# Kernel tuning notes

Measured on AMD Instinct MI355X. Metric: run time of the kernel, lower is better.

Reference implementation:

```python
import jax, jax.numpy as jnp
import numpy as np

N_PER_CLOUD = 2048   # points per cloud (batch entries are equal-sized, sorted)
NUM_CLOUDS = 8       # batch_size constant in the source module
RADIUS = 0.2         # init arg r
MAX_NEIGHBORS = 32   # init arg max_neighbors
F_IN, H1, H2, F_OUT = 3, 64, 64, 128  # PointNet++ SA MLP widths; nn input = F_IN + 3


def setup_inputs() -> dict:
    key = jax.random.key(0)
    ks = jax.random.split(key, 8)
    N = NUM_CLOUDS * N_PER_CLOUD
    x = jax.random.normal(ks[0], (N, F_IN), dtype=jnp.float32)
    pos = jax.random.uniform(ks[1], (N, 3), dtype=jnp.float32)  # unit cube
    batch = jnp.repeat(jnp.arange(NUM_CLOUDS, dtype=jnp.int32), N_PER_CLOUD)
    d_in = F_IN + 3
    W1 = jax.random.normal(ks[2], (d_in, H1), dtype=jnp.float32) / np.sqrt(d_in)
    b1 = jnp.zeros((H1,), dtype=jnp.float32)
    W2 = jax.random.normal(ks[3], (H1, H2), dtype=jnp.float32) / np.sqrt(H1)
    b2 = jnp.zeros((H2,), dtype=jnp.float32)
    W3 = jax.random.normal(ks[4], (H2, F_OUT), dtype=jnp.float32) / np.sqrt(H2)
    b3 = jnp.zeros((F_OUT,), dtype=jnp.float32)
    return dict(x=x, pos=pos, batch=batch, W1=W1, b1=b1, W2=W2, b2=b2, W3=W3, b3=b3)


def reference(x, pos, batch, W1, b1, W2, b2, W3, b3):
    N = pos.shape[0]
    B = N // N_PER_CLOUD
    n = N_PER_CLOUD
    posb = pos.reshape(B, n, 3)
    xb = x.reshape(B, n, -1)

    # --- radius ball query (per cloud, first MAX_NEIGHBORS in index order) ---
    diff = posb[:, :, None, :] - posb[:, None, :, :]          # [B, n_query, n_src, 3]
    d2 = jnp.sum(diff * diff, axis=-1)                        # [B, n, n]
    valid = d2 <= RADIUS * RADIUS                             # includes self -> >=1 nbr
    j_idx = jnp.arange(n, dtype=jnp.int32)
    keys = jnp.where(valid, j_idx[None, None, :], n)          # invalid -> sentinel n
    nbr = jnp.argsort(keys, axis=-1)[..., :MAX_NEIGHBORS]     # [B, n, K]
    nbr_ok = jnp.take_along_axis(keys, nbr, axis=-1) < n      # [B, n, K] bool

    # --- PointNetConv: msg = nn(cat([x_j, pos_j - pos_i])), max aggregation ---
    b_ix = jnp.arange(B)[:, None, None]
    x_j = xb[b_ix, nbr]                                        # [B, n, K, F_IN]
    rel = posb[b_ix, nbr] - posb[:, :, None, :]               # [B, n, K, 3]
    msg = jnp.concatenate([x_j, rel], axis=-1)                # [B, n, K, F_IN+3]
    h = jax.nn.relu(msg @ W1 + b1)
    h = jax.nn.relu(h @ W2 + b2)
    h = h @ W3 + b3                                           # [B, n, K, F_OUT]
    h = jnp.where(nbr_ok[..., None], h, -jnp.inf)
    out = jnp.max(h, axis=2).reshape(N, -1)                   # [N, F_OUT]
    return out, pos, batch
```

## Files before the change

kernel.cpp:

```cpp
#include <hip/hip_runtime.h>
#include <hip/hip_bf16.h>
#include <math.h>

#define NPC   2048
#define NC    8
#define NTOT  (NPC * NC)
#define KMAX  32
#define R2    0.04f

typedef short bf16x8  __attribute__((ext_vector_type(8)));
typedef float f32x16  __attribute__((ext_vector_type(16)));

__device__ __forceinline__ unsigned int f2bf(float f) {
    unsigned int u = __float_as_uint(f);
    return (u + 0x7FFFu + ((u >> 16) & 1u)) >> 16;
}

__device__ __forceinline__ unsigned int pkbf(float a, float b) {
    unsigned int r;
    asm("v_cvt_pk_bf16_f32 %0, %1, %2" : "=v"(r) : "v"(a), "v"(b));
    return r;
}

__device__ __forceinline__ bf16x8 mk_frag(const f32x16& a, int off) {
    int4 w;
    w.x = (int)pkbf(fmaxf(a[off+0],0.f), fmaxf(a[off+1],0.f));
    w.y = (int)pkbf(fmaxf(a[off+2],0.f), fmaxf(a[off+3],0.f));
    w.z = (int)pkbf(fmaxf(a[off+4],0.f), fmaxf(a[off+5],0.f));
    w.w = (int)pkbf(fmaxf(a[off+6],0.f), fmaxf(a[off+7],0.f));
    return __builtin_bit_cast(bf16x8, w);
}

__global__ __launch_bounds__(512) void prep_kernel(
    const float* __restrict__ x, const float* __restrict__ pos,
    const int* __restrict__ batch,
    const float* __restrict__ W1, const float* __restrict__ b1,
    const float* __restrict__ W2, const float* __restrict__ b2,
    const float* __restrict__ W3,
    int* __restrict__ nbr, int* __restrict__ cnts,
    float* __restrict__ xp, unsigned short* __restrict__ wf,
    float* __restrict__ out)
{
    __shared__ float4 sP[NPC];

    int b = blockIdx.x, tid = threadIdx.x;
    if (b < 2048) {
        const int base = (b >> 8) << 11;
        #pragma unroll
        for (int p = tid; p < NPC; p += 512) {
            sP[p] = make_float4(pos[3*(base+p)], pos[3*(base+p)+1], pos[3*(base+p)+2], 0.f);
        }
        __syncthreads();

        const int lane = tid & 63;
        const int q    = b * 8 + (tid >> 6);
        float qx = pos[3*q], qy = pos[3*q+1], qz = pos[3*q+2];
        int cnt = 0;
        for (int j0 = 0; j0 < NPC && cnt < KMAX; j0 += 256) {
            unsigned long long ms[4];
            bool vs[4];
            #pragma unroll
            for (int s = 0; s < 4; ++s) {
                float4 p = sP[j0 + s*64 + lane];
                float dx = __fsub_rn(p.x, qx);
                float dy = __fsub_rn(p.y, qy);
                float dz = __fsub_rn(p.z, qz);
                float d2 = __fadd_rn(__fadd_rn(__fmul_rn(dx,dx), __fmul_rn(dy,dy)),
                                     __fmul_rn(dz,dz));
                vs[s] = d2 <= R2;
                ms[s] = __ballot(vs[s]);
            }
            #pragma unroll
            for (int s = 0; s < 4; ++s) {
                int before = (int)__popcll(ms[s] & ((1ull << lane) - 1ull));
                int slot = cnt + before;
                if (vs[s] && slot < KMAX) nbr[(q << 5) + slot] = base + j0 + s*64 + lane;
                cnt += (int)__popcll(ms[s]);
            }
        }
        if (lane == 0) cnts[q] = cnt < KMAX ? cnt : KMAX;
    } else if (b < 2080) {
        int i = (b - 2048) * 512 + tid;
        float4 v0 = {x[3*i], x[3*i+1], x[3*i+2], pos[3*i]};
        float4 v1 = {pos[3*i+1], pos[3*i+2], 0.f, 0.f};
        float4* dst = (float4*)(xp + 8 * i);
        dst[0] = v0; dst[1] = v1;
    } else if (b < 2108) {
        int g = (b - 2080) * 512 + tid;
        if (g < 1024) {
            int j = g & 7, lane = (g >> 3) & 63, t = g >> 9;
            int k = (lane >> 5)*8 + j, ch = t*32 + (lane & 31);
            float v = (k < 6) ? W1[k*64 + ch] : (k == 6 ? b1[ch] : 0.f);
            wf[g] = (unsigned short)f2bf(v);
        } else if (g < 6144) {
            int g2 = g - 1024;
            int j = g2 & 7, lane = (g2 >> 3) & 63, f = g2 >> 9;
            int t = f / 5, kk = f % 5;
            int hi = lane >> 5, row = t*32 + (lane & 31);
            float v;
            if (kk < 4) {
                int k = (j & 3) + 4*hi + 8*(2*(kk & 1) + (j >> 2)) + 32*(kk >> 1);
                v = W2[k*64 + row];
            } else {
                v = (hi == 0 && j == 0) ? b2[row] : 0.f;
            }
            wf[g] = (unsigned short)f2bf(v);
        } else {
            int g3 = g - 6144;
            int j = g3 & 7, lane = (g3 >> 3) & 63, f = g3 >> 9;
            int n = f >> 2, kk = f & 3;
            int hi = lane >> 5, col = n*32 + (lane & 31);
            int k = (j & 3) + 4*hi + 8*(2*(kk & 1) + (j >> 2)) + 32*(kk >> 1);
            wf[g] = (unsigned short)f2bf(W3[k*128 + col]);
        }
    } else {
        int i = (b - 2108) * 512 + tid;
        if (i < NTOT*3) out[NTOT*128 + i] = pos[i];
        if (i < NTOT)   out[NTOT*131 + i] = (float)batch[i];
    }
}

__global__ __launch_bounds__(256, 4) void mlp_kernel(
    const unsigned short* __restrict__ wf, const float* __restrict__ b3,
    const float* __restrict__ xp,
    const int* __restrict__ nbr, const int* __restrict__ cnts,
    float* __restrict__ out)
{
    __shared__ int4 sW[1664];

    const int tid  = threadIdx.x;
    const int lane = tid & 63, wave = tid >> 6;
    const int e = lane & 31, hi = lane >> 5;

    const int qq  = __builtin_amdgcn_readfirstlane(blockIdx.x * 4 + wave);
    const int cnt = cnts[qq];

    int jg = (e < cnt) ? nbr[(qq << 5) + e] : qq;
    const float4* pj = (const float4*)(xp + 8*jg);
    float4 xj0 = pj[0], xj1 = pj[1];
    float qpx = xp[8*qq + 3], qpy = xp[8*qq + 4], qpz = xp[8*qq + 5];

    bf16x8 wA1_0 = *(const bf16x8*)(wf + (0*64 + lane)*8);
    bf16x8 wA1_1 = *(const bf16x8*)(wf + (1*64 + lane)*8);

    float b3v[4];
    #pragma unroll
    for (int n = 0; n < 4; ++n) b3v[n] = b3[n*32 + e];

    const int4* wsrc = (const int4*)(wf + 1024);
    #pragma unroll
    for (int it = 0; it < 7; ++it) {
        int idx = it*256 + tid;
        if (idx < 1664) sW[idx] = wsrc[idx];
    }
    __syncthreads();

    const unsigned int one_w = pkbf(1.0f, 0.0f);
    int4 ow = {0,0,0,0};
    if (!hi) ow.x = (int)one_w;
    const bf16x8 onef = __builtin_bit_cast(bf16x8, ow);

    float r0 = xj0.w - qpx, r1 = xj1.x - qpy, r2 = xj1.y - qpz;
    int4 mw;
    mw.x = hi ? 0 : (int)pkbf(xj0.x, xj0.y);
    mw.y = hi ? 0 : (int)pkbf(xj0.z, r0);
    mw.z = hi ? 0 : (int)pkbf(r1, r2);
    mw.w = hi ? 0 : (int)one_w;
    bf16x8 msgf = __builtin_bit_cast(bf16x8, mw);

    f32x16 acc0 = {}, acc1 = {};
    acc0 = __builtin_amdgcn_mfma_f32_32x32x16_bf16(wA1_0, msgf, acc0, 0, 0, 0);
    acc1 = __builtin_amdgcn_mfma_f32_32x32x16_bf16(wA1_1, msgf, acc1, 0, 0, 0);
    bf16x8 h1f[4];
    h1f[0] = mk_frag(acc0, 0);
    h1f[1] = mk_frag(acc0, 8);
    h1f[2] = mk_frag(acc1, 0);
    h1f[3] = mk_frag(acc1, 8);

    f32x16 c20 = {}, c21 = {};
    #pragma unroll
    for (int kk = 0; kk < 4; ++kk) {
        c20 = __builtin_amdgcn_mfma_f32_32x32x16_bf16(
                *(const bf16x8*)&sW[(0*5 + kk)*64 + lane], h1f[kk], c20, 0, 0, 0);
        c21 = __builtin_amdgcn_mfma_f32_32x32x16_bf16(
                *(const bf16x8*)&sW[(1*5 + kk)*64 + lane], h1f[kk], c21, 0, 0, 0);
    }
    c20 = __builtin_amdgcn_mfma_f32_32x32x16_bf16(
            *(const bf16x8*)&sW[(0*5 + 4)*64 + lane], onef, c20, 0, 0, 0);
    c21 = __builtin_amdgcn_mfma_f32_32x32x16_bf16(
            *(const bf16x8*)&sW[(1*5 + 4)*64 + lane], onef, c21, 0, 0, 0);
    bf16x8 h2f[4];
    h2f[0] = mk_frag(c20, 0);
    h2f[1] = mk_frag(c20, 8);
    h2f[2] = mk_frag(c21, 0);
    h2f[3] = mk_frag(c21, 8);

    const bool full = (cnt == 32);
    #pragma unroll
    for (int n = 0; n < 4; ++n) {
        f32x16 c = {};
        #pragma unroll
        for (int kk = 0; kk < 4; ++kk)
            c = __builtin_amdgcn_mfma_f32_32x32x16_bf16(
                    h2f[kk], *(const bf16x8*)&sW[640 + (n*4 + kk)*64 + lane], c, 0, 0, 0);
        float m;
        if (full) {
            m = fmaxf(fmaxf(fmaxf(c[0],c[1]), fmaxf(c[2],c[3])),
                      fmaxf(fmaxf(c[4],c[5]), fmaxf(c[6],c[7])));
            m = fmaxf(m, fmaxf(fmaxf(c[8],c[9]),  fmaxf(c[10],c[11])));
            m = fmaxf(m, fmaxf(fmaxf(c[12],c[13]), fmaxf(c[14],c[15])));
        } else {
            m = -INFINITY;
            #pragma unroll
            for (int reg = 0; reg < 16; ++reg) {
                int r = (reg & 3) + 8*(reg >> 2) + 4*hi;
                float v = (r < cnt) ? c[reg] : -INFINITY;
                m = fmaxf(m, v);
            }
        }
        m = fmaxf(m, __shfl_xor(m, 32));
        m += b3v[n];
        if (hi == 0) out[qq*128 + n*32 + (lane & 31)] = m;
    }
}

extern "C" void kernel_launch(void* const* d_in, const int* in_sizes, int n_in,
                              void* d_out, int out_size, void* d_ws, size_t ws_size,
                              hipStream_t stream) {
    const float* x     = (const float*)d_in[0];
    const float* pos   = (const float*)d_in[1];
    const int*   batch = (const int*)d_in[2];
    const float* W1    = (const float*)d_in[3];
    const float* b1    = (const float*)d_in[4];
    const float* W2    = (const float*)d_in[5];
    const float* b2    = (const float*)d_in[6];
    const float* W3    = (const float*)d_in[7];
    const float* b3    = (const float*)d_in[8];
    float* out = (float*)d_out;

    int* nbr  = (int*)d_ws;
    int* cnts = nbr + NTOT * KMAX;
    float* xp = (float*)(cnts + NTOT);
    unsigned short* wfrag = (unsigned short*)(xp + NTOT*8);

    prep_kernel<<<2204, 512, 0, stream>>>(x, pos, batch, W1, b1, W2, b2, W3,
                                          nbr, cnts, xp, wfrag, out);
    mlp_kernel<<<NTOT / 4, 256, 0, stream>>>(wfrag, b3, xp, nbr, cnts, out);
}
```

Baseline: 38.44 us.

## Process two query points per wave to reuse weight fragments across MFMAs

Each wave now handles two query points instead of one. Every weight fragment loaded from LDS or global memory feeds two independent MFMA chains, and the grid is halved, so the per-block shared-memory weight staging is amortised over twice the work. The extra accumulators raise register pressure, so the launch-bounds occupancy hint drops from 4 to 3, which may reduce latency hiding.

Measured after the change: 36.75 us. 4.4% less time.

```diff
diff --git a/kernel.cpp b/kernel.cpp
--- a/kernel.cpp
+++ b/kernel.cpp
@@ -120,7 +120,7 @@
     }
 }
 
-__global__ __launch_bounds__(256, 4) void mlp_kernel(
+__global__ __launch_bounds__(256, 3) void mlp_kernel(
     const unsigned short* __restrict__ wf, const float* __restrict__ b3,
     const float* __restrict__ xp,
     const int* __restrict__ nbr, const int* __restrict__ cnts,
@@ -132,13 +132,16 @@
     const int lane = tid & 63, wave = tid >> 6;
     const int e = lane & 31, hi = lane >> 5;
 
-    const int qq  = __builtin_amdgcn_readfirstlane(blockIdx.x * 4 + wave);
-    const int cnt = cnts[qq];
-
-    int jg = (e < cnt) ? nbr[(qq << 5) + e] : qq;
-    const float4* pj = (const float4*)(xp + 8*jg);
-    float4 xj0 = pj[0], xj1 = pj[1];
-    float qpx = xp[8*qq + 3], qpy = xp[8*qq + 4], qpz = xp[8*qq + 5];
+    const int q0 = __builtin_amdgcn_readfirstlane(blockIdx.x * 8 + wave * 2);
+    const int q1 = q0 + 1;
+    const int cnt0 = cnts[q0], cnt1 = cnts[q1];
+
+    int jg0 = (e < cnt0) ? nbr[(q0 << 5) + e] : q0;
+    int jg1 = (e < cnt1) ? nbr[(q1 << 5) + e] : q1;
+    float4 a0 = ((const float4*)(xp + 8*jg0))[0], a1 = ((const float4*)(xp + 8*jg0))[1];
+    float4 c0 = ((const float4*)(xp + 8*jg1))[0], c1 = ((const float4*)(xp + 8*jg1))[1];
+    float p0x = xp[8*q0 + 3], p0y = xp[8*q0 + 4], p0z = xp[8*q0 + 5];
+    float p1x = xp[8*q1 + 3], p1y = xp[8*q1 + 4], p1z = xp[8*q1 + 5];
 
     bf16x8 wA1_0 = *(const bf16x8*)(wf + (0*64 + lane)*8);
     bf16x8 wA1_1 = *(const bf16x8*)(wf + (1*64 + lane)*8);
@@ -160,67 +163,96 @@
     if (!hi) ow.x = (int)one_w;
     const bf16x8 onef = __builtin_bit_cast(bf16x8, ow);
 
-    float r0 = xj0.w - qpx, r1 = xj1.x - qpy, r2 = xj1.y - qpz;
-    int4 mw;
-    mw.x = hi ? 0 : (int)pkbf(xj0.x, xj0.y);
-    mw.y = hi ? 0 : (int)pkbf(xj0.z, r0);
-    mw.z = hi ? 0 : (int)pkbf(r1, r2);
-    mw.w = hi ? 0 : (int)one_w;
-    bf16x8 msgf = __builtin_bit_cast(bf16x8, mw);
-
-    f32x16 acc0 = {}, acc1 = {};
-    acc0 = __builtin_amdgcn_mfma_f32_32x32x16_bf16(wA1_0, msgf, acc0, 0, 0, 0);
-    acc1 = __builtin_amdgcn_mfma_f32_32x32x16_bf16(wA1_1, msgf, acc1, 0, 0, 0);
-    bf16x8 h1f[4];
-    h1f[0] = mk_frag(acc0, 0);
-    h1f[1] = mk_frag(acc0, 8);
-    h1f[2] = mk_frag(acc1, 0);
-    h1f[3] = mk_frag(acc1, 8);
-
-    f32x16 c20 = {}, c21 = {};
+    int4 mw0, mw1;
+    mw0.x = hi ? 0 : (int)pkbf(a0.x, a0.y);
+    mw0.y = hi ? 0 : (int)pkbf(a0.z, a0.w - p0x);
+    mw0.z = hi ? 0 : (int)pkbf(a1.x - p0y, a1.y - p0z);
+    mw0.w = hi ? 0 : (int)one_w;
+    mw1.x = hi ? 0 : (int)pkbf(c0.x, c0.y);
+    mw1.y = hi ? 0 : (int)pkbf(c0.z, c0.w - p1x);
+    mw1.z = hi ? 0 : (int)pkbf(c1.x - p1y, c1.y - p1z);
+    mw1.w = hi ? 0 : (int)one_w;
+    bf16x8 msg0 = __builtin_bit_cast(bf16x8, mw0);
+    bf16x8 msg1 = __builtin_bit_cast(bf16x8, mw1);
+
+    f32x16 l0a = {}, l0b = {}, l1a = {}, l1b = {};
+    l0a = __builtin_amdgcn_mfma_f32_32x32x16_bf16(wA1_0, msg0, l0a, 0, 0, 0);
+    l1a = __builtin_amdgcn_mfma_f32_32x32x16_bf16(wA1_0, msg1, l1a, 0, 0, 0);
+    l0b = __builtin_amdgcn_mfma_f32_32x32x16_bf16(wA1_1, msg0, l0b, 0, 0, 0);
+    l1b = __builtin_amdgcn_mfma_f32_32x32x16_bf16(wA1_1, msg1, l1b, 0, 0, 0);
+    bf16x8 h1f0[4], h1f1[4];
+    h1f0[0] = mk_frag(l0a, 0); h1f0[1] = mk_frag(l0a, 8);
+    h1f0[2] = mk_frag(l0b, 0); h1f0[3] = mk_frag(l0b, 8);
+    h1f1[0] = mk_frag(l1a, 0); h1f1[1] = mk_frag(l1a, 8);
+    h1f1[2] = mk_frag(l1b, 0); h1f1[3] = mk_frag(l1b, 8);
+
+    f32x16 g0a = {}, g0b = {}, g1a = {}, g1b = {};
     #pragma unroll
     for (int kk = 0; kk < 4; ++kk) {
-        c20 = __builtin_amdgcn_mfma_f32_32x32x16_bf16(
-                *(const bf16x8*)&sW[(0*5 + kk)*64 + lane], h1f[kk], c20, 0, 0, 0);
-        c21 = __builtin_amdgcn_mfma_f32_32x32x16_bf16(
-                *(const bf16x8*)&sW[(1*5 + kk)*64 + lane], h1f[kk], c21, 0, 0, 0);
-    }
-    c20 = __builtin_amdgcn_mfma_f32_32x32x16_bf16(
-            *(const bf16x8*)&sW[(0*5 + 4)*64 + lane], onef, c20, 0, 0, 0);
-    c21 = __builtin_amdgcn_mfma_f32_32x32x16_bf16(
-            *(const bf16x8*)&sW[(1*5 + 4)*64 + lane], onef, c21, 0, 0, 0);
-    bf16x8 h2f[4];
-    h2f[0] = mk_frag(c20, 0);
-    h2f[1] = mk_frag(c20, 8);
-    h2f[2] = mk_frag(c21, 0);
-    h2f[3] = mk_frag(c21, 8);
-
-    const bool full = (cnt == 32);
+        bf16x8 wa = *(const bf16x8*)&sW[(0*5 + kk)*64 + lane];
+        bf16x8 wb = *(const bf16x8*)&sW[(1*5 + kk)*64 + lane];
+        g0a = __builtin_amdgcn_mfma_f32_32x32x16_bf16(wa, h1f0[kk], g0a, 0, 0, 0);
+        g1a = __builtin_amdgcn_mfma_f32_32x32x16_bf16(wa, h1f1[kk], g1a, 0, 0, 0);
+        g0b = __builtin_amdgcn_mfma_f32_32x32x16_bf16(wb, h1f0[kk], g0b, 0, 0, 0);
+        g1b = __builtin_amdgcn_mfma_f32_32x32x16_bf16(wb, h1f1[kk], g1b, 0, 0, 0);
+    }
+    {
+        bf16x8 wa = *(const bf16x8*)&sW[(0*5 + 4)*64 + lane];
+        bf16x8 wb = *(const bf16x8*)&sW[(1*5 + 4)*64 + lane];
+        g0a = __builtin_amdgcn_mfma_f32_32x32x16_bf16(wa, onef, g0a, 0, 0, 0);
+        g1a = __builtin_amdgcn_mfma_f32_32x32x16_bf16(wa, onef, g1a, 0, 0, 0);
+        g0b = __builtin_amdgcn_mfma_f32_32x32x16_bf16(wb, onef, g0b, 0, 0, 0);
+        g1b = __builtin_amdgcn_mfma_f32_32x32x16_bf16(wb, onef, g1b, 0, 0, 0);
+    }
+    bf16x8 h2f0[4], h2f1[4];
+    h2f0[0] = mk_frag(g0a, 0); h2f0[1] = mk_frag(g0a, 8);
+    h2f0[2] = mk_frag(g0b, 0); h2f0[3] = mk_frag(g0b, 8);
+    h2f1[0] = mk_frag(g1a, 0); h2f1[1] = mk_frag(g1a, 8);
+    h2f1[2] = mk_frag(g1b, 0); h2f1[3] = mk_frag(g1b, 8);
+
+    const bool full0 = (cnt0 == 32), full1 = (cnt1 == 32);
     #pragma unroll
     for (int n = 0; n < 4; ++n) {
-        f32x16 c = {};
+        f32x16 v0 = {}, v1 = {};
         #pragma unroll
-        for (int kk = 0; kk < 4; ++kk)
-            c = __builtin_amdgcn_mfma_f32_32x32x16_bf16(
-                    h2f[kk], *(const bf16x8*)&sW[640 + (n*4 + kk)*64 + lane], c, 0, 0, 0);
-        float m;
-        if (full) {
-            m = fmaxf(fmaxf(fmaxf(c[0],c[1]), fmaxf(c[2],c[3])),
-                      fmaxf(fmaxf(c[4],c[5]), fmaxf(c[6],c[7])));
-            m = fmaxf(m, fmaxf(fmaxf(c[8],c[9]),  fmaxf(c[10],c[11])));
-            m = fmaxf(m, fmaxf(fmaxf(c[12],c[13]), fmaxf(c[14],c[15])));
+        for (int kk = 0; kk < 4; ++kk) {
+            bf16x8 bw = *(const bf16x8*)&sW[640 + (n*4 + kk)*64 + lane];
+            v0 = __builtin_amdgcn_mfma_f32_32x32x16_bf16(h2f0[kk], bw, v0, 0, 0, 0);
+            v1 = __builtin_amdgcn_mfma_f32_32x32x16_bf16(h2f1[kk], bw, v1, 0, 0, 0);
+        }
+        float m0, m1;
+        if (full0) {
+            m0 = fmaxf(fmaxf(fmaxf(v0[0],v0[1]), fmaxf(v0[2],v0[3])),
+                       fmaxf(fmaxf(v0[4],v0[5]), fmaxf(v0[6],v0[7])));
+            m0 = fmaxf(m0, fmaxf(fmaxf(v0[8],v0[9]),  fmaxf(v0[10],v0[11])));
+            m0 = fmaxf(m0, fmaxf(fmaxf(v0[12],v0[13]), fmaxf(v0[14],v0[15])));
         } else {
-            m = -INFINITY;
+            m0 = -INFINITY;
             #pragma unroll
             for (int reg = 0; reg < 16; ++reg) {
                 int r = (reg & 3) + 8*(reg >> 2) + 4*hi;
-                float v = (r < cnt) ? c[reg] : -INFINITY;
-                m = fmaxf(m, v);
-            }
-        }
-        m = fmaxf(m, __shfl_xor(m, 32));
-        m += b3v[n];
-        if (hi == 0) out[qq*128 + n*32 + (lane & 31)] = m;
+                m0 = fmaxf(m0, (r < cnt0) ? v0[reg] : -INFINITY);
+            }
+        }
+        if (full1) {
+            m1 = fmaxf(fmaxf(fmaxf(v1[0],v1[1]), fmaxf(v1[2],v1[3])),
+                       fmaxf(fmaxf(v1[4],v1[5]), fmaxf(v1[6],v1[7])));
+            m1 = fmaxf(m1, fmaxf(fmaxf(v1[8],v1[9]),  fmaxf(v1[10],v1[11])));
+            m1 = fmaxf(m1, fmaxf(fmaxf(v1[12],v1[13]), fmaxf(v1[14],v1[15])));
+        } else {
+            m1 = -INFINITY;
+            #pragma unroll
+            for (int reg = 0; reg < 16; ++reg) {
+                int r = (reg & 3) + 8*(reg >> 2) + 4*hi;
+                m1 = fmaxf(m1, (r < cnt1) ? v1[reg] : -INFINITY);
+            }
+        }
+        m0 = fmaxf(m0, __shfl_xor(m0, 32)) + b3v[n];
+        m1 = fmaxf(m1, __shfl_xor(m1, 32)) + b3v[n];
+        if (hi == 0) {
+            out[q0*128 + n*32 + e] = m0;
+            out[q1*128 + n*32 + e] = m1;
+        }
     }
 }
 
@@ -245,5 +277,5 @@
 
     prep_kernel<<<2204, 512, 0, stream>>>(x, pos, batch, W1, b1, W2, b2, W3,
                                           nbr, cnts, xp, wfrag, out);
-    mlp_kernel<<<NTOT / 4, 256, 0, stream>>>(wfrag, b3, xp, nbr, cnts, out);
-}
+    mlp_kernel<<<NTOT / 8, 256, 0, stream>>>(wfrag, b3, xp, nbr, cnts, out);
+}
```

## Fuse ball query into MLP kernel, keeping neighbor lists in shared memory

Applied to the files above, without the earlier changes.

The radius neighbor search moves from the prep kernel into the MLP kernel. Each 512-thread block loads its cloud's positions into shared memory, builds per-wave neighbor lists in LDS, then runs the MFMA MLP directly. This removes the global nbr/cnts/xp round trip and shrinks the prep kernel to weight packing and output copies. In exchange every block reloads 2048 positions plus the weights into LDS, and the bigger LDS footprint per block may cut occupancy.

Measured after the change: 43.34 us. 12.7% more time.

```diff
diff --git a/kernel.cpp b/kernel.cpp
--- a/kernel.cpp
+++ b/kernel.cpp
@@ -31,62 +31,16 @@
     return __builtin_bit_cast(bf16x8, w);
 }
 
-__global__ __launch_bounds__(512) void prep_kernel(
-    const float* __restrict__ x, const float* __restrict__ pos,
-    const int* __restrict__ batch,
+__global__ __launch_bounds__(512) void prep_small(
+    const float* __restrict__ pos, const int* __restrict__ batch,
     const float* __restrict__ W1, const float* __restrict__ b1,
     const float* __restrict__ W2, const float* __restrict__ b2,
     const float* __restrict__ W3,
-    int* __restrict__ nbr, int* __restrict__ cnts,
-    float* __restrict__ xp, unsigned short* __restrict__ wf,
-    float* __restrict__ out)
+    unsigned short* __restrict__ wf, float* __restrict__ out)
 {
-    __shared__ float4 sP[NPC];
-
     int b = blockIdx.x, tid = threadIdx.x;
-    if (b < 2048) {
-        const int base = (b >> 8) << 11;
-        #pragma unroll
-        for (int p = tid; p < NPC; p += 512) {
-            sP[p] = make_float4(pos[3*(base+p)], pos[3*(base+p)+1], pos[3*(base+p)+2], 0.f);
-        }
-        __syncthreads();
-
-        const int lane = tid & 63;
-        const int q    = b * 8 + (tid >> 6);
-        float qx = pos[3*q], qy = pos[3*q+1], qz = pos[3*q+2];
-        int cnt = 0;
-        for (int j0 = 0; j0 < NPC && cnt < KMAX; j0 += 256) {
-            unsigned long long ms[4];
-            bool vs[4];
-            #pragma unroll
-            for (int s = 0; s < 4; ++s) {
-                float4 p = sP[j0 + s*64 + lane];
-                float dx = __fsub_rn(p.x, qx);
-                float dy = __fsub_rn(p.y, qy);
-                float dz = __fsub_rn(p.z, qz);
-                float d2 = __fadd_rn(__fadd_rn(__fmul_rn(dx,dx), __fmul_rn(dy,dy)),
-                                     __fmul_rn(dz,dz));
-                vs[s] = d2 <= R2;
-                ms[s] = __ballot(vs[s]);
-            }
-            #pragma unroll
-            for (int s = 0; s < 4; ++s) {
-                int before = (int)__popcll(ms[s] & ((1ull << lane) - 1ull));
-                int slot = cnt + before;
-                if (vs[s] && slot < KMAX) nbr[(q << 5) + slot] = base + j0 + s*64 + lane;
-                cnt += (int)__popcll(ms[s]);
-            }
-        }
-        if (lane == 0) cnts[q] = cnt < KMAX ? cnt : KMAX;
-    } else if (b < 2080) {
-        int i = (b - 2048) * 512 + tid;
-        float4 v0 = {x[3*i], x[3*i+1], x[3*i+2], pos[3*i]};
-        float4 v1 = {pos[3*i+1], pos[3*i+2], 0.f, 0.f};
-        float4* dst = (float4*)(xp + 8 * i);
-        dst[0] = v0; dst[1] = v1;
-    } else if (b < 2108) {
-        int g = (b - 2080) * 512 + tid;
+    if (b < 28) {
+        int g = b * 512 + tid;
         if (g < 1024) {
             int j = g & 7, lane = (g >> 3) & 63, t = g >> 9;
             int k = (lane >> 5)*8 + j, ch = t*32 + (lane & 31);
@@ -114,56 +68,91 @@
             wf[g] = (unsigned short)f2bf(W3[k*128 + col]);
         }
     } else {
-        int i = (b - 2108) * 512 + tid;
+        int i = (b - 28) * 512 + tid;
         if (i < NTOT*3) out[NTOT*128 + i] = pos[i];
-        if (i < NTOT)   out[NTOT*131 + i] = (float)batch[i];
-    }
-}
-
-__global__ __launch_bounds__(256, 4) void mlp_kernel(
+        else            out[NTOT*131 + (i - NTOT*3)] = (float)batch[i - NTOT*3];
+    }
+}
+
+__global__ __launch_bounds__(512, 4) void fused_kernel(
+    const float* __restrict__ x, const float* __restrict__ pos,
     const unsigned short* __restrict__ wf, const float* __restrict__ b3,
-    const float* __restrict__ xp,
-    const int* __restrict__ nbr, const int* __restrict__ cnts,
     float* __restrict__ out)
 {
-    __shared__ int4 sW[1664];
+    __shared__ float4 sP[NPC];
+    __shared__ int4   sW[1664];
+    __shared__ int    snbr[8*32];
 
     const int tid  = threadIdx.x;
     const int lane = tid & 63, wave = tid >> 6;
     const int e = lane & 31, hi = lane >> 5;
-
-    const int qq  = __builtin_amdgcn_readfirstlane(blockIdx.x * 4 + wave);
-    const int cnt = cnts[qq];
-
-    int jg = (e < cnt) ? nbr[(qq << 5) + e] : qq;
-    const float4* pj = (const float4*)(xp + 8*jg);
-    float4 xj0 = pj[0], xj1 = pj[1];
-    float qpx = xp[8*qq + 3], qpy = xp[8*qq + 4], qpz = xp[8*qq + 5];
-
+    const int blk   = blockIdx.x;
+    const int base  = (blk >> 8) << 11;
+    const int q     = blk * 8 + wave;
+    const int ql    = q - base;
+
+    {
+        const float4* src = (const float4*)(pos + 3*base);
+        float4 f0 = src[3*tid], f1 = src[3*tid+1], f2 = src[3*tid+2];
+        sP[4*tid+0] = make_float4(f0.x, f0.y, f0.z, 0.f);
+        sP[4*tid+1] = make_float4(f0.w, f1.x, f1.y, 0.f);
+        sP[4*tid+2] = make_float4(f1.z, f1.w, f2.x, 0.f);
+        sP[4*tid+3] = make_float4(f2.y, f2.z, f2.w, 0.f);
+    }
+    const int4* wsrc = (const int4*)(wf + 1024);
+    #pragma unroll
+    for (int it = 0; it < 4; ++it) {
+        int idx = it*512 + tid;
+        if (idx < 1664) sW[idx] = wsrc[idx];
+    }
     bf16x8 wA1_0 = *(const bf16x8*)(wf + (0*64 + lane)*8);
     bf16x8 wA1_1 = *(const bf16x8*)(wf + (1*64 + lane)*8);
-
     float b3v[4];
     #pragma unroll
     for (int n = 0; n < 4; ++n) b3v[n] = b3[n*32 + e];
-
-    const int4* wsrc = (const int4*)(wf + 1024);
-    #pragma unroll
-    for (int it = 0; it < 7; ++it) {
-        int idx = it*256 + tid;
-        if (idx < 1664) sW[idx] = wsrc[idx];
-    }
     __syncthreads();
+
+    const float4 qp = sP[ql];
+    const float qx = qp.x, qy = qp.y, qz = qp.z;
+    int cnt = 0;
+    for (int j0 = 0; j0 < NPC && cnt < KMAX; j0 += 256) {
+        unsigned long long ms[4];
+        bool vs[4];
+        #pragma unroll
+        for (int s = 0; s < 4; ++s) {
+            float4 p = sP[j0 + s*64 + lane];
+            float dx = __fsub_rn(p.x, qx);
+            float dy = __fsub_rn(p.y, qy);
+            float dz = __fsub_rn(p.z, qz);
+            float d2 = __fadd_rn(__fadd_rn(__fmul_rn(dx,dx), __fmul_rn(dy,dy)),
+                                 __fmul_rn(dz,dz));
+            vs[s] = d2 <= R2;
+            ms[s] = __ballot(vs[s]);
+        }
+        #pragma unroll
+        for (int s = 0; s < 4; ++s) {
+            int before = (int)__popcll(ms[s] & ((1ull << lane) - 1ull));
+            int slot = cnt + before;
+            if (vs[s] && slot < KMAX) snbr[(wave << 5) + slot] = j0 + s*64 + lane;
+            cnt += (int)__popcll(ms[s]);
+        }
+    }
+    if (cnt > KMAX) cnt = KMAX;
+    __syncthreads();
+
+    int jl = (e < cnt) ? snbr[(wave << 5) + e] : ql;
+    float4 pj = sP[jl];
+    float xj0 = x[3*(base + jl)], xj1 = x[3*(base + jl) + 1], xj2 = x[3*(base + jl) + 2];
 
     const unsigned int one_w = pkbf(1.0f, 0.0f);
     int4 ow = {0,0,0,0};
     if (!hi) ow.x = (int)one_w;
     const bf16x8 onef = __builtin_bit_cast(bf16x8, ow);
 
-    float r0 = xj0.w - qpx, r1 = xj1.x - qpy, r2 = xj1.y - qpz;
+    float r0 = pj.x - qx, r1 = pj.y - qy, r2 = pj.z - qz;
     int4 mw;
-    mw.x = hi ? 0 : (int)pkbf(xj0.x, xj0.y);
-    mw.y = hi ? 0 : (int)pkbf(xj0.z, r0);
+    mw.x = hi ? 0 : (int)pkbf(xj0, xj1);
+    mw.y = hi ? 0 : (int)pkbf(xj2, r0);
     mw.z = hi ? 0 : (int)pkbf(r1, r2);
     mw.w = hi ? 0 : (int)one_w;
     bf16x8 msgf = __builtin_bit_cast(bf16x8, mw);
@@ -214,13 +203,12 @@
             #pragma unroll
             for (int reg = 0; reg < 16; ++reg) {
                 int r = (reg & 3) + 8*(reg >> 2) + 4*hi;
-                float v = (r < cnt) ? c[reg] : -INFINITY;
-                m = fmaxf(m, v);
+                m = fmaxf(m, (r < cnt) ? c[reg] : -INFINITY);
             }
         }
         m = fmaxf(m, __shfl_xor(m, 32));
         m += b3v[n];
-        if (hi == 0) out[qq*128 + n*32 + (lane & 31)] = m;
+        if (hi == 0) out[q*128 + n*32 + e] = m;
     }
 }
 
@@ -238,12 +226,8 @@
     const float* b3    = (const float*)d_in[8];
     float* out = (float*)d_out;
 
-    int* nbr  = (int*)d_ws;
-    int* cnts = nbr + NTOT * KMAX;
-    float* xp = (float*)(cnts + NTOT);
-    unsigned short* wfrag = (unsigned short*)(xp + NTOT*8);
-
-    prep_kernel<<<2204, 512, 0, stream>>>(x, pos, batch, W1, b1, W2, b2, W3,
-                                          nbr, cnts, xp, wfrag, out);
-    mlp_kernel<<<NTOT / 4, 256, 0, stream>>>(wfrag, b3, xp, nbr, cnts, out);
-}
+    unsigned short* wfrag = (unsigned short*)d_ws;
+
+    prep_small<<<156, 512, 0, stream>>>(pos, batch, W1, b1, W2, b2, W3, wfrag, out);
+    fused_kernel<<<2048, 512, 0, stream>>>(x, pos, wfrag, b3, out);
+}
```
